# Optimization experiments

Measured on AMD Instinct MI355X. Metric: run time of the kernel, lower is better.

The kernel has to match this reference:

```python
import jax, jax.numpy as jnp
import numpy as np

N = 10000      # nodes per graph-batch
E = 160000     # edges
G = 128        # number of graphs (segments)


def gcn_conv(x, edge_index, W, b, n):
    """PyG GCNConv with normalize=True, add_self_loops=True.
    x: [n, in], W: [in, out], b: [out], edge_index: [2, e]."""
    loops = jnp.arange(n, dtype=edge_index.dtype)
    src = jnp.concatenate([edge_index[0], loops])
    dst = jnp.concatenate([edge_index[1], loops])
    deg = jnp.zeros((n,), x.dtype).at[dst].add(1.0)          # in-degree incl. self-loops
    dinv = jnp.where(deg > 0, jax.lax.rsqrt(deg), 0.0)
    norm = dinv[src] * dinv[dst]                              # [e+n]
    h = x @ W                                                 # dense transform first
    out = jax.ops.segment_sum(norm[:, None] * h[src], dst, num_segments=n)
    return out + b


def global_max_pool(z, batch, g):
    p = jax.ops.segment_max(z, batch, num_segments=g)
    return jnp.where(jnp.isneginf(p), 0.0, p)  # guard empty segments


def setup_inputs() -> dict:
    key = jax.random.key(0)
    ks = jax.random.split(key, 24)

    def w(k, i, o):
        return (jax.random.normal(k, (i, o), jnp.float32) / np.sqrt(i)).astype(jnp.float32)

    inp = {
        "x_s": jax.random.normal(ks[0], (N, 128), jnp.float32),
        "x_t": jax.random.normal(ks[1], (N, 128), jnp.float32),
        "edge_index_s": jax.random.randint(ks[2], (2, E), 0, N, dtype=jnp.int32),
        "edge_index_t": jax.random.randint(ks[3], (2, E), 0, N, dtype=jnp.int32),
        "xs_batch": jnp.sort(jax.random.randint(ks[4], (N,), 0, G, dtype=jnp.int32)),
        "xt_batch": jnp.sort(jax.random.randint(ks[5], (N,), 0, G, dtype=jnp.int32)),
        # encoder GCNConvs (128 -> 512)
        "W_enc1": w(ks[6], 128, 512), "b_enc1": jnp.zeros((512,), jnp.float32),
        "W_enc2": w(ks[7], 128, 512), "b_enc2": jnp.zeros((512,), jnp.float32),
        # branch-1 GCNConvs
        "W_r1g1": w(ks[8], 512, 1024), "b_r1g1": jnp.zeros((1024,), jnp.float32),
        "W_r1g2": w(ks[9], 1024, 2048), "b_r1g2": jnp.zeros((2048,), jnp.float32),
        # branch-2 GCNConvs
        "W_r2g1": w(ks[10], 512, 1024), "b_r2g1": jnp.zeros((1024,), jnp.float32),
        "W_r2g2": w(ks[11], 1024, 2048), "b_r2g2": jnp.zeros((2048,), jnp.float32),
        # MLP head
        "W_l1": w(ks[12], 2048, 1024), "b_l1": jnp.zeros((1024,), jnp.float32),
        "W_l2": w(ks[13], 1024, 1317), "b_l2": jnp.zeros((1317,), jnp.float32),
    }
    return inp


def reference(x_s, x_t, W_enc1, b_enc1, W_enc2, b_enc2,
              W_r1g1, b_r1g1, W_r1g2, b_r1g2,
              W_r2g1, b_r2g1, W_r2g2, b_r2g2,
              W_l1, b_l1, W_l2, b_l2,
              edge_index_s, edge_index_t, xs_batch, xt_batch):
    # branch 1 (source graphs)
    enc_r1 = gcn_conv(x_s, edge_index_s, W_enc1, b_enc1, N)
    z_r1 = jax.nn.relu(gcn_conv(enc_r1, edge_index_s, W_r1g1, b_r1g1, N))
    z_r1 = jax.nn.relu(gcn_conv(z_r1, edge_index_s, W_r1g2, b_r1g2, N))
    # branch 2 (target graphs)
    enc_r2 = gcn_conv(x_t, edge_index_t, W_enc2, b_enc2, N)
    z_r2 = jax.nn.relu(gcn_conv(enc_r2, edge_index_t, W_r2g1, b_r2g1, N))
    z_r2 = jax.nn.relu(gcn_conv(z_r2, edge_index_t, W_r2g2, b_r2g2, N))
    # global max pool per graph, then MLP head
    z = global_max_pool(z_r1, xs_batch, G) + global_max_pool(z_r2, xt_batch, G)  # [G, 2048]
    z = jax.nn.relu(z @ W_l1 + b_l1)
    z = z @ W_l2 + b_l2                                                          # [G, 1317]
    return (z, jax.nn.sigmoid(z))
```

## Files before the change

kernel.cpp:

```cpp
#include <hip/hip_runtime.h>
#include <cstdint>
#include <cstddef>


#define NN 10000
#define NNP 10112
#define MT 20224
#define NB 632
#define NE 160000
#define NG 128

typedef short bf16x8 __attribute__((ext_vector_type(8)));
typedef float f32x4 __attribute__((ext_vector_type(4)));

__device__ __forceinline__ unsigned short f2bf(float x) {
  unsigned u = __float_as_uint(x);
  u += 0x7FFFu + ((u >> 16) & 1u);
  return (unsigned short)(u >> 16);
}
__device__ __forceinline__ float bf2f(unsigned short h) {
  return __uint_as_float(((unsigned)h) << 16);
}
__device__ __forceinline__ void fma4(float4& d, float s, const float4& u) {
  d.x = fmaf(s, u.x, d.x);
  d.y = fmaf(s, u.y, d.y);
  d.z = fmaf(s, u.z, d.z);
  d.w = fmaf(s, u.w, d.w);
}

#define GLOAD_LDS16(gp, lp)                                                  \
  __builtin_amdgcn_global_load_lds(                                          \
      (const __attribute__((address_space(1))) void*)(gp),                   \
      (__attribute__((address_space(3))) void*)(lp), 16, 0, 0)


__global__ void k_count2(const int* __restrict__ eis, const int* __restrict__ eit,
                         int* __restrict__ cnt) {
  int i = blockIdx.x * blockDim.x + threadIdx.x;
  if (i >= 2 * NE) return;
  int d;
  if (i < NE) d = eis[NE + i];
  else        d = eit[NE + (i - NE)] + NNP;
  atomicAdd(&cnt[d], 1);
}

__global__ void k_scan(const int* __restrict__ cnt, int* __restrict__ row_ptr,
                       int* __restrict__ cursor, float* __restrict__ dinv,
                       const int* __restrict__ bs, const int* __restrict__ bt,
                       int* __restrict__ seg) {
  __shared__ int part[256];
  __shared__ int partex[257];
  int t = threadIdx.x;
  const int n = MT;
  const int CH = (n + 255) / 256;
  int base = t * CH;
  int s = 0;
  for (int i = 0; i < CH; ++i) {
    int idx = base + i;
    if (idx < n) s += cnt[idx];
  }
  part[t] = s;
  __syncthreads();
  if (t == 0) {
    int acc = 0;
    for (int i = 0; i < 256; ++i) { partex[i] = acc; acc += part[i]; }
    partex[256] = acc;
  }
  __syncthreads();
  int acc = partex[t];
  for (int i = 0; i < CH; ++i) {
    int idx = base + i;
    if (idx < n) {
      row_ptr[idx] = acc;
      cursor[idx]  = acc;
      dinv[idx] = rsqrtf((float)cnt[idx] + 1.0f);
      acc += cnt[idx];
    }
  }
  if (t == 255) row_ptr[n] = partex[256];
  if (t <= NG) {
    int lo = 0, hi = NN;
    while (lo < hi) {
      int mid = (lo + hi) >> 1;
      if (bs[mid] < t) lo = mid + 1;
      else hi = mid;
    }
    seg[t] = lo;
    lo = 0; hi = NN;
    while (lo < hi) {
      int mid = (lo + hi) >> 1;
      if (bt[mid] < t) lo = mid + 1;
      else hi = mid;
    }
    seg[(NG + 1) + t] = lo;
  }
}

__global__ void k_scatter2(const int* __restrict__ eis, const int* __restrict__ eit,
                           int* __restrict__ cursor, int* __restrict__ csr_src) {
  int i = blockIdx.x * blockDim.x + threadIdx.x;
  if (i >= 2 * NE) return;
  int s, d;
  if (i < NE) { s = eis[i]; d = eis[NE + i]; }
  else { int j = i - NE; s = eit[j] + NNP; d = eit[NE + j] + NNP; }
  int pos = atomicAdd(&cursor[d], 1);
  csr_src[pos] = s;
}

template <int NCH, bool DUAL>
__global__ __launch_bounds__(256) void k_agg_x(
    const float* __restrict__ in0, const float* __restrict__ in1,
    unsigned short* __restrict__ Ah, unsigned short* __restrict__ Al,
    const int* __restrict__ row_ptr, const int* __restrict__ csr_src,
    const float* __restrict__ dinv) {
  constexpr int F4TOT = NCH * 8;
  const int bid = blockIdx.x;
  const int xcd = bid & 7;
  const int seq = bid >> 3;
  int chunk, nodeblk;
  if constexpr (NCH >= 8) {
    int phase = seq / NB;
    nodeblk = seq - phase * NB;
    chunk = phase * 8 + xcd;
  } else {
    chunk = xcd >> 1;
    nodeblk = (seq << 1) | (xcd & 1);
  }
  const int t = threadIdx.x;
  const int node = nodeblk * 32 + (t >> 3);
  const int f4 = chunk * 8 + (t & 7);

  size_t o = (size_t)node * F4TOT + f4;
  ushort4* oh = (ushort4*)Ah + o;
  ushort4* ol = (ushort4*)Al + o;
  int local = (node < NNP) ? node : (node - NNP);
  if (local >= NN) {
    *oh = make_ushort4(0, 0, 0, 0);
    *ol = make_ushort4(0, 0, 0, 0);
    return;
  }
  const float4* i0 = (const float4*)in0;
  const float4* i1 = (const float4*)in1;
  auto rowp = [&](int g) -> const float4* {
    if (DUAL)
      return (g < NNP) ? (i0 + (size_t)g * F4TOT)
                       : (i1 + (size_t)(g - NNP) * F4TOT);
    return i0 + (size_t)g * F4TOT;
  };

  float di = dinv[node];
  float sw = di * di;
  float4 v = rowp(node)[f4];
  float4 acc;
  acc.x = sw * v.x; acc.y = sw * v.y; acc.z = sw * v.z; acc.w = sw * v.w;

  const int e0 = row_ptr[node], e1 = row_ptr[node + 1];
  int e = e0;
  for (; e + 4 <= e1; e += 4) {
    int s0 = csr_src[e], s1 = csr_src[e + 1];
    int s2 = csr_src[e + 2], s3 = csr_src[e + 3];
    float4 u0 = rowp(s0)[f4];
    float4 u1 = rowp(s1)[f4];
    float4 u2 = rowp(s2)[f4];
    float4 u3 = rowp(s3)[f4];
    float w0 = dinv[s0] * di, w1 = dinv[s1] * di;
    float w2 = dinv[s2] * di, w3 = dinv[s3] * di;
    fma4(acc, w0, u0);
    fma4(acc, w1, u1);
    fma4(acc, w2, u2);
    fma4(acc, w3, u3);
  }
  for (; e < e1; ++e) {
    int s = csr_src[e];
    float4 u = rowp(s)[f4];
    fma4(acc, dinv[s] * di, u);
  }

  ushort4 h, l;
  h.x = f2bf(acc.x); l.x = f2bf(acc.x - bf2f(h.x));
  h.y = f2bf(acc.y); l.y = f2bf(acc.y - bf2f(h.y));
  h.z = f2bf(acc.z); l.z = f2bf(acc.z - bf2f(h.z));
  h.w = f2bf(acc.w); l.w = f2bf(acc.w - bf2f(h.w));
  *oh = h;
  *ol = l;
}

__global__ __launch_bounds__(256) void k_wsplit2(
    const float* __restrict__ W0, unsigned short* __restrict__ H0,
    unsigned short* __restrict__ L0,
    const float* __restrict__ W1, unsigned short* __restrict__ H1,
    unsigned short* __restrict__ L1, int K, int N) {
  const float* W = blockIdx.z ? W1 : W0;
  unsigned short* Ht = blockIdx.z ? H1 : H0;
  unsigned short* Lt = blockIdx.z ? L1 : L0;
  __shared__ float tile[32][33];
  int nb = blockIdx.x * 32, kb = blockIdx.y * 32;
  int tx = threadIdx.x & 31, ty = threadIdx.x >> 5;
#pragma unroll
  for (int r = ty; r < 32; r += 8)
    tile[r][tx] = W[(size_t)(kb + r) * N + nb + tx];
  __syncthreads();
#pragma unroll
  for (int r = ty; r < 32; r += 8) {
    float x = tile[tx][r];
    unsigned short h = f2bf(x);
    unsigned short lo = f2bf(x - bf2f(h));
    size_t o = (size_t)(nb + r) * K + kb + tx;
    Ht[o] = h;
    Lt[o] = lo;
  }
}

template <bool RELU, int GX>
__global__ __launch_bounds__(256) void k_mgemm(
    const unsigned short* __restrict__ Ah, const unsigned short* __restrict__ Al,
    const unsigned short* __restrict__ Bh_a, const unsigned short* __restrict__ Bl_a,
    const unsigned short* __restrict__ Bh_b, const unsigned short* __restrict__ Bl_b,
    const float* __restrict__ bias_a, const float* __restrict__ bias_b,
    float* __restrict__ C, int N, int K, int AOFF) {
  __shared__ char smem[65536];
  const int t = threadIdx.x;
  const int w = t >> 6, l = t & 63;

  const int bid = blockIdx.x;
  int bn_, bm_;
  if constexpr (GX == 16) { bn_ = 2 * (bid & 7) + ((bid >> 3) & 1); bm_ = bid >> 4; }
  else if constexpr (GX == 8) { bn_ = bid & 7; bm_ = bid >> 3; }
  else { bn_ = bid & (GX - 1); bm_ = bid / GX; }
  const int bm = bm_ * 128, bn = bn_ * 128;
  const int arow = bm + AOFF;
  const bool sec = arow >= NNP;
  const unsigned short* Bh = sec ? Bh_b : Bh_a;
  const unsigned short* Bl = sec ? Bl_b : Bl_a;
  const float* bias = sec ? bias_b : bias_a;

  const int wr = w >> 1, wc = w & 1;

  f32x4 acc[4][4] = {};

  const unsigned short* g0 = (w == 0) ? Ah : (w == 1) ? Al : (w == 2) ? Bh : Bl;
  const int rb = (w < 2) ? arow : bn;
  const unsigned short* gbase = g0 + (size_t)(rb + (l & 15)) * K + ((l >> 4) * 8);
  const int sdoff = w * 8192 + l * 16;
  const int saoff = wr * 4096 + l * 16;
  const int sboff = 16384 + wc * 4096 + l * 16;

  const int nt = K >> 5;

#define STAGE(kt, b)                                                         \
  {                                                                          \
    const unsigned short* gk = gbase + ((kt) << 5);                          \
    char* sd = smem + (b)*32768 + sdoff;                                     \
    _Pragma("unroll") for (int s = 0; s < 8; ++s)                            \
        GLOAD_LDS16(gk + (size_t)s * 16 * K, sd + s * 1024);                 \
  }

  STAGE(0, 0)

  for (int kt = 0; kt < nt; ++kt) {
    const int cur = kt & 1;
    if (kt + 1 < nt) {
      STAGE(kt + 1, cur ^ 1)
      asm volatile("s_waitcnt vmcnt(8)" ::: "memory");
    } else {
      asm volatile("s_waitcnt vmcnt(0)" ::: "memory");
    }
    __builtin_amdgcn_sched_barrier(0);
    __builtin_amdgcn_s_barrier();

    const char* sA = smem + cur * 32768 + saoff;
    const char* sB = smem + cur * 32768 + sboff;
    bf16x8 a[4][2], b[4][2];
#pragma unroll
    for (int i = 0; i < 4; ++i) {
      a[i][0] = *(const bf16x8*)(sA + i * 1024);
      a[i][1] = *(const bf16x8*)(sA + 8192 + i * 1024);
    }
#pragma unroll
    for (int j = 0; j < 4; ++j) {
      b[j][0] = *(const bf16x8*)(sB + j * 1024);
      b[j][1] = *(const bf16x8*)(sB + 8192 + j * 1024);
    }
    asm volatile("s_waitcnt lgkmcnt(0)" ::: "memory");
    __builtin_amdgcn_sched_barrier(0);
    __builtin_amdgcn_s_barrier();

    __builtin_amdgcn_s_setprio(1);
#pragma unroll
    for (int i = 0; i < 4; ++i)
#pragma unroll
      for (int j = 0; j < 4; ++j) {
        acc[i][j] = __builtin_amdgcn_mfma_f32_16x16x32_bf16(a[i][0], b[j][0], acc[i][j], 0, 0, 0);
        acc[i][j] = __builtin_amdgcn_mfma_f32_16x16x32_bf16(a[i][0], b[j][1], acc[i][j], 0, 0, 0);
        acc[i][j] = __builtin_amdgcn_mfma_f32_16x16x32_bf16(a[i][1], b[j][0], acc[i][j], 0, 0, 0);
      }
    __builtin_amdgcn_s_setprio(0);
  }
#undef STAGE

  const int r0 = bm + wr * 64 + ((l >> 4) << 2);
  const int c0 = bn + wc * 64 + (l & 15);
#pragma unroll
  for (int j = 0; j < 4; ++j) {
    const int col = c0 + j * 16;
    const float bv = bias[col];
#pragma unroll
    for (int i = 0; i < 4; ++i) {
      const int row = r0 + i * 16;
#pragma unroll
      for (int r = 0; r < 4; ++r) {
        float v = acc[i][j][r] + bv;
        if (RELU) v = fmaxf(v, 0.f);
        C[(size_t)(row + r) * N + col] = v;
      }
    }
  }
}

__global__ __launch_bounds__(256) void k_gemm_sk(
    const float* __restrict__ A, const float* __restrict__ A2,
    const float* __restrict__ B,
    float* __restrict__ PART, int M, int N, int K, int KS) {
  __shared__ float As[32][64];
  __shared__ float Bs[32][64];

  int t = threadIdx.x;
  int tx = t & 15, ty = t >> 4;
  int bm = blockIdx.y * 64, bn = blockIdx.x * 64;
  int kbeg = blockIdx.z * KS, kend = kbeg + KS;

  float acc[4][4] = {};

  int arow0 = t >> 3;
  int ak4 = (t & 7) * 4;
  int brow0 = t >> 4;
  int bn4 = (t & 15) * 4;
  const bool n4al = (N & 3) == 0;

  for (int k0 = kbeg; k0 < kend; k0 += 32) {
#pragma unroll
    for (int c = 0; c < 2; ++c) {
      int row = arow0 + c * 32;
      int gr = bm + row;
      float4 v = make_float4(0.f, 0.f, 0.f, 0.f);
      if (gr < M) {
        v = *(const float4*)&A[(size_t)gr * K + k0 + ak4];
        if (A2) {
          float4 v2 = *(const float4*)&A2[(size_t)gr * K + k0 + ak4];
          v.x += v2.x; v.y += v2.y; v.z += v2.z; v.w += v2.w;
        }
      }
      As[ak4 + 0][row] = v.x;
      As[ak4 + 1][row] = v.y;
      As[ak4 + 2][row] = v.z;
      As[ak4 + 3][row] = v.w;
    }
#pragma unroll
    for (int c = 0; c < 2; ++c) {
      int row = brow0 + c * 16;
      int gc = bn + bn4;
      const float* bp = &B[(size_t)(k0 + row) * N + gc];
      float4 v;
      if (n4al && gc + 3 < N) {
        v = *(const float4*)bp;
      } else {
        v = make_float4(0.f, 0.f, 0.f, 0.f);
        if (gc < N) v.x = bp[0];
        if (gc + 1 < N) v.y = bp[1];
        if (gc + 2 < N) v.z = bp[2];
        if (gc + 3 < N) v.w = bp[3];
      }
      *(float4*)&Bs[row][bn4] = v;
    }
    __syncthreads();

#pragma unroll
    for (int kk = 0; kk < 32; ++kk) {
      float4 a = *(const float4*)&As[kk][ty * 4];
      float4 b = *(const float4*)&Bs[kk][tx * 4];
      float av[4] = {a.x, a.y, a.z, a.w};
      float bv[4] = {b.x, b.y, b.z, b.w};
#pragma unroll
      for (int i = 0; i < 4; ++i)
#pragma unroll
        for (int j = 0; j < 4; ++j)
          acc[i][j] = fmaf(av[i], bv[j], acc[i][j]);
    }
    __syncthreads();
  }

  float* P = PART + (size_t)blockIdx.z * M * N;
  int r0 = bm + ty * 4, c0 = bn + tx * 4;
#pragma unroll
  for (int i = 0; i < 4; ++i) {
    int r = r0 + i;
    if (r < M) {
#pragma unroll
      for (int j = 0; j < 4; ++j) {
        int c = c0 + j;
        if (c < N) P[(size_t)r * N + c] = acc[i][j];
      }
    }
  }
}

template <bool SIG>
__global__ void k_reduce(const float* __restrict__ PART,
                         const float* __restrict__ bias,
                         float* __restrict__ C, float* __restrict__ C2,
                         int MN, int N, int SK) {
  int i = blockIdx.x * blockDim.x + threadIdx.x;
  if (i >= MN) return;
  float s = 0.f;
  for (int z = 0; z < SK; ++z) s += PART[(size_t)z * MN + i];
  s += bias[i % N];
  if (SIG) {
    C[i] = s;
    C2[i] = 1.0f / (1.0f + __expf(-s));
  } else {
    C[i] = fmaxf(s, 0.f);
  }
}


__global__ void k_pool(const float* __restrict__ act, const int* __restrict__ segp,
                       float* __restrict__ P, int F4) {
  int g = blockIdx.x;
  int f4 = blockIdx.y * blockDim.x + threadIdx.x;
  if (f4 >= F4) return;
  const float4* a4 = (const float4*)act;
  int i0 = segp[g], i1 = segp[g + 1];
  float4 m = make_float4(0.f, 0.f, 0.f, 0.f);
  for (int i = i0; i < i1; ++i) {
    float4 u = a4[(size_t)i * F4 + f4];
    m.x = fmaxf(m.x, u.x);
    m.y = fmaxf(m.y, u.y);
    m.z = fmaxf(m.z, u.z);
    m.w = fmaxf(m.w, u.w);
  }
  ((float4*)P)[(size_t)g * F4 + f4] = m;
}


extern "C" void kernel_launch(void* const* d_in, const int* in_sizes, int n_in,
                              void* d_out, int out_size, void* d_ws, size_t ws_size,
                              hipStream_t stream) {
  const float* x_s = (const float*)d_in[0];
  const float* x_t = (const float*)d_in[1];
  const int* ei_s = (const int*)d_in[2];
  const int* ei_t = (const int*)d_in[3];
  const int* xs_batch = (const int*)d_in[4];
  const int* xt_batch = (const int*)d_in[5];
  const float* W_enc1 = (const float*)d_in[6];
  const float* b_enc1 = (const float*)d_in[7];
  const float* W_enc2 = (const float*)d_in[8];
  const float* b_enc2 = (const float*)d_in[9];
  const float* W_r1g1 = (const float*)d_in[10];
  const float* b_r1g1 = (const float*)d_in[11];
  const float* W_r1g2 = (const float*)d_in[12];
  const float* b_r1g2 = (const float*)d_in[13];
  const float* W_r2g1 = (const float*)d_in[14];
  const float* b_r2g1 = (const float*)d_in[15];
  const float* W_r2g2 = (const float*)d_in[16];
  const float* b_r2g2 = (const float*)d_in[17];
  const float* W_l1 = (const float*)d_in[18];
  const float* b_l1 = (const float*)d_in[19];
  const float* W_l2 = (const float*)d_in[20];
  const float* b_l2 = (const float*)d_in[21];

  float* out = (float*)d_out;

  char* ws = (char*)d_ws;
  size_t off = 0;
  auto carve = [&](size_t bytes) {
    char* p = ws + off;
    off = (off + bytes + 255) & ~(size_t)255;
    return p;
  };
  float* ACT = (float*)carve((size_t)MT * 1024 * 4);
  float* ACT3 = ACT;
  unsigned short* Ah = (unsigned short*)carve((size_t)MT * 1024 * 2);
  unsigned short* Al = (unsigned short*)carve((size_t)MT * 1024 * 2);
  unsigned short* W1h_a = (unsigned short*)carve((size_t)512 * 128 * 2);
  unsigned short* W1l_a = (unsigned short*)carve((size_t)512 * 128 * 2);
  unsigned short* W1h_b = (unsigned short*)carve((size_t)512 * 128 * 2);
  unsigned short* W1l_b = (unsigned short*)carve((size_t)512 * 128 * 2);
  unsigned short* W2h_a = (unsigned short*)carve((size_t)1024 * 512 * 2);
  unsigned short* W2l_a = (unsigned short*)carve((size_t)1024 * 512 * 2);
  unsigned short* W2h_b = (unsigned short*)carve((size_t)1024 * 512 * 2);
  unsigned short* W2l_b = (unsigned short*)carve((size_t)1024 * 512 * 2);
  unsigned short* W3h_a = (unsigned short*)carve((size_t)2048 * 1024 * 2);
  unsigned short* W3l_a = (unsigned short*)carve((size_t)2048 * 1024 * 2);
  unsigned short* W3h_b = (unsigned short*)carve((size_t)2048 * 1024 * 2);
  unsigned short* W3l_b = (unsigned short*)carve((size_t)2048 * 1024 * 2);
  float* P2   = (float*)carve((size_t)2 * NG * 2048 * 4);
  float* ZZ   = (float*)carve((size_t)NG * 1024 * 4);
  float* PART = (float*)carve((size_t)16 * NG * 1024 * 4);
  float* dinv = (float*)carve((size_t)MT * 4);
  int* cnt     = (int*)carve((size_t)MT * 4);
  int* row_ptr = (int*)carve((size_t)(MT + 1) * 4);
  int* cursor  = (int*)carve((size_t)MT * 4);
  int* csr_src = (int*)carve((size_t)2 * NE * 4);
  int* seg     = (int*)carve((size_t)2 * (NG + 1) * 4);
  (void)ws_size; (void)n_in; (void)in_sizes; (void)out_size;

  k_wsplit2<<<dim3(512 / 32, 128 / 32, 2), 256, 0, stream>>>(
      W_enc1, W1h_a, W1l_a, W_enc2, W1h_b, W1l_b, 128, 512);
  k_wsplit2<<<dim3(1024 / 32, 512 / 32, 2), 256, 0, stream>>>(
      W_r1g1, W2h_a, W2l_a, W_r2g1, W2h_b, W2l_b, 512, 1024);
  k_wsplit2<<<dim3(2048 / 32, 1024 / 32, 2), 256, 0, stream>>>(
      W_r1g2, W3h_a, W3l_a, W_r2g2, W3h_b, W3l_b, 1024, 2048);

  hipMemsetAsync(cnt, 0, (size_t)MT * 4, stream);
  k_count2<<<(2 * NE + 255) / 256, 256, 0, stream>>>(ei_s, ei_t, cnt);
  k_scan<<<1, 256, 0, stream>>>(cnt, row_ptr, cursor, dinv, xs_batch, xt_batch, seg);
  k_scatter2<<<(2 * NE + 255) / 256, 256, 0, stream>>>(ei_s, ei_t, cursor, csr_src);

  k_agg_x<4, true><<<NB * 4, 256, 0, stream>>>(
      x_s, x_t, Ah, Al, row_ptr, csr_src, dinv);
  k_mgemm<false, 4><<<4 * (MT / 128), 256, 0, stream>>>(
      Ah, Al, W1h_a, W1l_a, W1h_b, W1l_b, b_enc1, b_enc2, ACT, 512, 128, 0);

  k_agg_x<16, false><<<NB * 16, 256, 0, stream>>>(
      ACT, nullptr, Ah, Al, row_ptr, csr_src, dinv);
  k_mgemm<true, 8><<<8 * (MT / 128), 256, 0, stream>>>(
      Ah, Al, W2h_a, W2l_a, W2h_b, W2l_b, b_r1g1, b_r2g1, ACT, 1024, 512, 0);

  k_agg_x<32, false><<<NB * 32, 256, 0, stream>>>(
      ACT, nullptr, Ah, Al, row_ptr, csr_src, dinv);
  k_mgemm<true, 16><<<16 * (NNP / 128), 256, 0, stream>>>(
      Ah, Al, W3h_a, W3l_a, W3h_b, W3l_b, b_r1g2, b_r2g2, ACT3, 2048, 1024, 0);
  k_pool<<<dim3(NG, 2), 256, 0, stream>>>(ACT3, seg, P2, 512);
  k_mgemm<true, 16><<<16 * (NNP / 128), 256, 0, stream>>>(
      Ah, Al, W3h_a, W3l_a, W3h_b, W3l_b, b_r1g2, b_r2g2, ACT3, 2048, 1024, NNP);
  k_pool<<<dim3(NG, 2), 256, 0, stream>>>(ACT3, seg + (NG + 1),
                                          P2 + (size_t)NG * 2048, 512);

  k_gemm_sk<<<dim3(1024 / 64, 2, 16), 256, 0, stream>>>(
      P2, P2 + (size_t)NG * 2048, W_l1, PART, NG, 1024, 2048, 128);
  k_reduce<false><<<(NG * 1024 + 255) / 256, 256, 0, stream>>>(
      PART, b_l1, ZZ, nullptr, NG * 1024, 1024, 16);

  const int OUTN = 1317;
  k_gemm_sk<<<dim3((OUTN + 63) / 64, 2, 8), 256, 0, stream>>>(
      ZZ, nullptr, W_l2, PART, NG, OUTN, 1024, 128);
  k_reduce<true><<<(NG * OUTN + 255) / 256, 256, 0, stream>>>(
      PART, b_l2, out, out + (size_t)NG * OUTN, NG * OUTN, OUTN, 8);
}
```

Baseline: 835.2 us.

## Stage only hi bf16 halves in LDS; load lo halves directly from global

The split-bf16 GEMM now stages only the high halves of A and B in shared memory and halves the LDS footprint. The low halves are read straight from global memory into registers by each wave. The hand-tuned waitcnt, sched_barrier and setprio pipeline is replaced with plain __syncthreads. This aims to raise occupancy and cut LDS traffic, but the uncoalesced-ish per-wave global loads of lo halves and the coarser synchronisation could expose memory latency.

```diff
diff --git a/kernel.cpp b/kernel.cpp
--- a/kernel.cpp
+++ b/kernel.cpp
@@ -218,7 +218,7 @@
     const unsigned short* __restrict__ Bh_b, const unsigned short* __restrict__ Bl_b,
     const float* __restrict__ bias_a, const float* __restrict__ bias_b,
     float* __restrict__ C, int N, int K, int AOFF) {
-  __shared__ char smem[65536];
+  __shared__ char smem[32768];
   const int t = threadIdx.x;
   const int w = t >> 6, l = t & 63;
 
@@ -238,63 +238,59 @@
 
   f32x4 acc[4][4] = {};
 
-  const unsigned short* g0 = (w == 0) ? Ah : (w == 1) ? Al : (w == 2) ? Bh : Bl;
-  const int rb = (w < 2) ? arow : bn;
-  const unsigned short* gbase = g0 + (size_t)(rb + (l & 15)) * K + ((l >> 4) * 8);
-  const int sdoff = w * 8192 + l * 16;
+  const unsigned short* gmat = (w < 2) ? Ah : Bh;
+  const int rb0 = ((w < 2) ? arow : bn) + (w & 1) * 64;
+  const unsigned short* gsbase = gmat + (size_t)(rb0 + (l & 15)) * K + ((l >> 4) * 8);
+  const int sdoff = ((w < 2) ? 0 : 8192) + (w & 1) * 4096 + l * 16;
+
   const int saoff = wr * 4096 + l * 16;
-  const int sboff = 16384 + wc * 4096 + l * 16;
+  const int sboff = 8192 + wc * 4096 + l * 16;
+
+  const unsigned short* gal = Al + (size_t)(arow + wr * 64 + (l & 15)) * K + ((l >> 4) * 8);
+  const unsigned short* gbl = Bl + (size_t)(bn + wc * 64 + (l & 15)) * K + ((l >> 4) * 8);
 
   const int nt = K >> 5;
 
 #define STAGE(kt, b)                                                         \
   {                                                                          \
-    const unsigned short* gk = gbase + ((kt) << 5);                          \
-    char* sd = smem + (b)*32768 + sdoff;                                     \
-    _Pragma("unroll") for (int s = 0; s < 8; ++s)                            \
-        GLOAD_LDS16(gk + (size_t)s * 16 * K, sd + s * 1024);                 \
+    _Pragma("unroll") for (int s = 0; s < 4; ++s)                            \
+        GLOAD_LDS16(gsbase + (size_t)s * 16 * K + ((kt) << 5),               \
+                    smem + (b)*16384 + sdoff + s * 1024);                    \
   }
 
   STAGE(0, 0)
+  __syncthreads();
 
   for (int kt = 0; kt < nt; ++kt) {
     const int cur = kt & 1;
-    if (kt + 1 < nt) {
-      STAGE(kt + 1, cur ^ 1)
-      asm volatile("s_waitcnt vmcnt(8)" ::: "memory");
-    } else {
-      asm volatile("s_waitcnt vmcnt(0)" ::: "memory");
-    }
-    __builtin_amdgcn_sched_barrier(0);
-    __builtin_amdgcn_s_barrier();
-
-    const char* sA = smem + cur * 32768 + saoff;
-    const char* sB = smem + cur * 32768 + sboff;
-    bf16x8 a[4][2], b[4][2];
-#pragma unroll
-    for (int i = 0; i < 4; ++i) {
-      a[i][0] = *(const bf16x8*)(sA + i * 1024);
-      a[i][1] = *(const bf16x8*)(sA + 8192 + i * 1024);
-    }
-#pragma unroll
-    for (int j = 0; j < 4; ++j) {
-      b[j][0] = *(const bf16x8*)(sB + j * 1024);
-      b[j][1] = *(const bf16x8*)(sB + 8192 + j * 1024);
-    }
-    asm volatile("s_waitcnt lgkmcnt(0)" ::: "memory");
-    __builtin_amdgcn_sched_barrier(0);
-    __builtin_amdgcn_s_barrier();
-
-    __builtin_amdgcn_s_setprio(1);
+    if (kt + 1 < nt) STAGE(kt + 1, cur ^ 1)
+
+    const int k0 = kt << 5;
+    bf16x8 alo[4], blo[4];
 #pragma unroll
     for (int i = 0; i < 4; ++i)
+      alo[i] = *(const bf16x8*)(gal + (size_t)(i * 16) * K + k0);
+#pragma unroll
+    for (int j = 0; j < 4; ++j)
+      blo[j] = *(const bf16x8*)(gbl + (size_t)(j * 16) * K + k0);
+
+    const char* sA = smem + cur * 16384 + saoff;
+    const char* sB = smem + cur * 16384 + sboff;
+    bf16x8 ahi[4], bhi[4];
+#pragma unroll
+    for (int i = 0; i < 4; ++i) ahi[i] = *(const bf16x8*)(sA + i * 1024);
+#pragma unroll
+    for (int j = 0; j < 4; ++j) bhi[j] = *(const bf16x8*)(sB + j * 1024);
+
+#pragma unroll
+    for (int i = 0; i < 4; ++i)
 #pragma unroll
       for (int j = 0; j < 4; ++j) {
-        acc[i][j] = __builtin_amdgcn_mfma_f32_16x16x32_bf16(a[i][0], b[j][0], acc[i][j], 0, 0, 0);
-        acc[i][j] = __builtin_amdgcn_mfma_f32_16x16x32_bf16(a[i][0], b[j][1], acc[i][j], 0, 0, 0);
-        acc[i][j] = __builtin_amdgcn_mfma_f32_16x16x32_bf16(a[i][1], b[j][0], acc[i][j], 0, 0, 0);
+        acc[i][j] = __builtin_amdgcn_mfma_f32_16x16x32_bf16(ahi[i], bhi[j], acc[i][j], 0, 0, 0);
+        acc[i][j] = __builtin_amdgcn_mfma_f32_16x16x32_bf16(ahi[i], blo[j], acc[i][j], 0, 0, 0);
+        acc[i][j] = __builtin_amdgcn_mfma_f32_16x16x32_bf16(alo[i], bhi[j], acc[i][j], 0, 0, 0);
       }
-    __builtin_amdgcn_s_setprio(0);
+    __syncthreads();
   }
 #undef STAGE
 
```

Result: slower. 1.013 ms (+21.3%).

## Fuse final GCN GEMM with global max pool via atomicMax, 256x256 tiles

Applied to the files above, without the earlier changes.

Replaces the two half-size final-layer GEMM launches and their separate pool kernels with a single 256x256-tile, 512-thread GEMM. Its epilogue applies bias and ReLU, then atomically max-reduces into the pooled buffer using integer atomicMax on non-negative floats, so the 20k x 2048 activation is never written to or re-read from global memory. Node padding rises to 10240 so the larger tiles divide the rows, and the segment binary search in the scan kernel is dropped. The cost is atomic contention on the pooled buffer, a memset, some extra padded rows of work, and higher LDS and register pressure per block.

```diff
diff --git a/kernel.cpp b/kernel.cpp
--- a/kernel.cpp
+++ b/kernel.cpp
@@ -4,9 +4,9 @@
 
 
 #define NN 10000
-#define NNP 10112
-#define MT 20224
-#define NB 632
+#define NNP2 10240
+#define MT2 20480
+#define NB2 640
 #define NE 160000
 #define NG 128
 
@@ -40,25 +40,20 @@
   if (i >= 2 * NE) return;
   int d;
   if (i < NE) d = eis[NE + i];
-  else        d = eit[NE + (i - NE)] + NNP;
+  else        d = eit[NE + (i - NE)] + NNP2;
   atomicAdd(&cnt[d], 1);
 }
 
 __global__ void k_scan(const int* __restrict__ cnt, int* __restrict__ row_ptr,
-                       int* __restrict__ cursor, float* __restrict__ dinv,
-                       const int* __restrict__ bs, const int* __restrict__ bt,
-                       int* __restrict__ seg) {
+                       int* __restrict__ cursor, float* __restrict__ dinv) {
   __shared__ int part[256];
   __shared__ int partex[257];
   int t = threadIdx.x;
-  const int n = MT;
-  const int CH = (n + 255) / 256;
+  const int n = MT2;
+  const int CH = n / 256;
   int base = t * CH;
   int s = 0;
-  for (int i = 0; i < CH; ++i) {
-    int idx = base + i;
-    if (idx < n) s += cnt[idx];
-  }
+  for (int i = 0; i < CH; ++i) s += cnt[base + i];
   part[t] = s;
   __syncthreads();
   if (t == 0) {
@@ -70,30 +65,12 @@
   int acc = partex[t];
   for (int i = 0; i < CH; ++i) {
     int idx = base + i;
-    if (idx < n) {
-      row_ptr[idx] = acc;
-      cursor[idx]  = acc;
-      dinv[idx] = rsqrtf((float)cnt[idx] + 1.0f);
-      acc += cnt[idx];
-    }
+    row_ptr[idx] = acc;
+    cursor[idx]  = acc;
+    dinv[idx] = rsqrtf((float)cnt[idx] + 1.0f);
+    acc += cnt[idx];
   }
   if (t == 255) row_ptr[n] = partex[256];
-  if (t <= NG) {
-    int lo = 0, hi = NN;
-    while (lo < hi) {
-      int mid = (lo + hi) >> 1;
-      if (bs[mid] < t) lo = mid + 1;
-      else hi = mid;
-    }
-    seg[t] = lo;
-    lo = 0; hi = NN;
-    while (lo < hi) {
-      int mid = (lo + hi) >> 1;
-      if (bt[mid] < t) lo = mid + 1;
-      else hi = mid;
-    }
-    seg[(NG + 1) + t] = lo;
-  }
 }
 
 __global__ void k_scatter2(const int* __restrict__ eis, const int* __restrict__ eit,
@@ -102,7 +79,7 @@
   if (i >= 2 * NE) return;
   int s, d;
   if (i < NE) { s = eis[i]; d = eis[NE + i]; }
-  else { int j = i - NE; s = eit[j] + NNP; d = eit[NE + j] + NNP; }
+  else { int j = i - NE; s = eit[j] + NNP2; d = eit[NE + j] + NNP2; }
   int pos = atomicAdd(&cursor[d], 1);
   csr_src[pos] = s;
 }
@@ -119,8 +96,8 @@
   const int seq = bid >> 3;
   int chunk, nodeblk;
   if constexpr (NCH >= 8) {
-    int phase = seq / NB;
-    nodeblk = seq - phase * NB;
+    int phase = seq / NB2;
+    nodeblk = seq - phase * NB2;
     chunk = phase * 8 + xcd;
   } else {
     chunk = xcd >> 1;
@@ -133,7 +110,7 @@
   size_t o = (size_t)node * F4TOT + f4;
   ushort4* oh = (ushort4*)Ah + o;
   ushort4* ol = (ushort4*)Al + o;
-  int local = (node < NNP) ? node : (node - NNP);
+  int local = (node < NNP2) ? node : (node - NNP2);
   if (local >= NN) {
     *oh = make_ushort4(0, 0, 0, 0);
     *ol = make_ushort4(0, 0, 0, 0);
@@ -143,8 +120,8 @@
   const float4* i1 = (const float4*)in1;
   auto rowp = [&](int g) -> const float4* {
     if (DUAL)
-      return (g < NNP) ? (i0 + (size_t)g * F4TOT)
-                       : (i1 + (size_t)(g - NNP) * F4TOT);
+      return (g < NNP2) ? (i0 + (size_t)g * F4TOT)
+                        : (i1 + (size_t)(g - NNP2) * F4TOT);
     return i0 + (size_t)g * F4TOT;
   };
 
@@ -217,19 +194,15 @@
     const unsigned short* __restrict__ Bh_a, const unsigned short* __restrict__ Bl_a,
     const unsigned short* __restrict__ Bh_b, const unsigned short* __restrict__ Bl_b,
     const float* __restrict__ bias_a, const float* __restrict__ bias_b,
-    float* __restrict__ C, int N, int K, int AOFF) {
+    float* __restrict__ C, int N, int K) {
   __shared__ char smem[65536];
   const int t = threadIdx.x;
   const int w = t >> 6, l = t & 63;
 
   const int bid = blockIdx.x;
-  int bn_, bm_;
-  if constexpr (GX == 16) { bn_ = 2 * (bid & 7) + ((bid >> 3) & 1); bm_ = bid >> 4; }
-  else if constexpr (GX == 8) { bn_ = bid & 7; bm_ = bid >> 3; }
-  else { bn_ = bid & (GX - 1); bm_ = bid / GX; }
+  const int bn_ = bid & (GX - 1), bm_ = bid / GX;
   const int bm = bm_ * 128, bn = bn_ * 128;
-  const int arow = bm + AOFF;
-  const bool sec = arow >= NNP;
+  const bool sec = bm >= NNP2;
   const unsigned short* Bh = sec ? Bh_b : Bh_a;
   const unsigned short* Bl = sec ? Bl_b : Bl_a;
   const float* bias = sec ? bias_b : bias_a;
@@ -239,7 +212,7 @@
   f32x4 acc[4][4] = {};
 
   const unsigned short* g0 = (w == 0) ? Ah : (w == 1) ? Al : (w == 2) ? Bh : Bl;
-  const int rb = (w < 2) ? arow : bn;
+  const int rb = (w < 2) ? bm : bn;
   const unsigned short* gbase = g0 + (size_t)(rb + (l & 15)) * K + ((l >> 4) * 8);
   const int sdoff = w * 8192 + l * 16;
   const int saoff = wr * 4096 + l * 16;
@@ -312,6 +285,132 @@
         float v = acc[i][j][r] + bv;
         if (RELU) v = fmaxf(v, 0.f);
         C[(size_t)(row + r) * N + col] = v;
+      }
+    }
+  }
+}
+
+__global__ __launch_bounds__(512, 2) void k_mgemm3(
+    const unsigned short* __restrict__ Ah, const unsigned short* __restrict__ Al,
+    const unsigned short* __restrict__ Bh_a, const unsigned short* __restrict__ Bl_a,
+    const unsigned short* __restrict__ Bh_b, const unsigned short* __restrict__ Bl_b,
+    const float* __restrict__ bias_a, const float* __restrict__ bias_b,
+    const int* __restrict__ bs, const int* __restrict__ bt,
+    float* __restrict__ P2, int N, int K) {
+  __shared__ char smem[131072];
+  const int t = threadIdx.x;
+  const int w = t >> 6, l = t & 63;
+  const int bid = blockIdx.x;
+  const int bn_ = bid & 7, bm_ = bid >> 3;
+  const int bm = bm_ * 256, bn = bn_ * 256;
+  const bool sec = bm >= NNP2;
+  const unsigned short* Bh = sec ? Bh_b : Bh_a;
+  const unsigned short* Bl = sec ? Bl_b : Bl_a;
+  const float* bias = sec ? bias_b : bias_a;
+  const int* batch = sec ? bt : bs;
+  float* P2g = P2 + (sec ? (size_t)NG * 2048 : 0);
+  const int lbase = bm - (sec ? NNP2 : 0);
+
+  const int wr = w >> 2, wc = w & 3;
+
+  f32x4 acc[8][4] = {};
+
+  const int part = w >> 1, half = w & 1;
+  const unsigned short* gmat = (part == 0) ? Ah : (part == 1) ? Al
+                             : (part == 2) ? Bh : Bl;
+  const int rb = ((part < 2) ? bm : bn) + half * 128;
+  const unsigned short* gsbase = gmat + (size_t)(rb + (l & 15)) * K + ((l >> 4) * 8);
+  const int sdoff = part * 16384 + half * 8192 + l * 16;
+
+  const int saoff = (wr * 8) * 1024 + l * 16;
+  const int sboff = 32768 + (wc * 4) * 1024 + l * 16;
+
+  const int nt = K >> 5;
+
+#define STAGE3(kt, b)                                                        \
+  {                                                                          \
+    _Pragma("unroll") for (int c = 0; c < 8; ++c)                            \
+        GLOAD_LDS16(gsbase + (size_t)c * 16 * K + ((kt) << 5),               \
+                    smem + (b)*65536 + sdoff + c * 1024);                    \
+  }
+
+  STAGE3(0, 0)
+
+  for (int kt = 0; kt < nt; ++kt) {
+    const int cur = kt & 1;
+    if (kt + 1 < nt) {
+      STAGE3(kt + 1, cur ^ 1)
+      asm volatile("s_waitcnt vmcnt(8)" ::: "memory");
+    } else {
+      asm volatile("s_waitcnt vmcnt(0)" ::: "memory");
+    }
+    __builtin_amdgcn_sched_barrier(0);
+    __builtin_amdgcn_s_barrier();
+
+    const char* base = smem + cur * 65536;
+    bf16x8 bh[4], blo[4], ah[8], alo[8];
+#pragma unroll
+    for (int j = 0; j < 4; ++j) {
+      bh[j]  = *(const bf16x8*)(base + sboff + j * 1024);
+      blo[j] = *(const bf16x8*)(base + sboff + 16384 + j * 1024);
+    }
+#pragma unroll
+    for (int i = 0; i < 8; ++i) {
+      ah[i]  = *(const bf16x8*)(base + saoff + i * 1024);
+      alo[i] = *(const bf16x8*)(base + saoff + 16384 + i * 1024);
+    }
+    asm volatile("s_waitcnt lgkmcnt(0)" ::: "memory");
+    __builtin_amdgcn_sched_barrier(0);
+    __builtin_amdgcn_s_barrier();
+
+    __builtin_amdgcn_s_setprio(1);
+#pragma unroll
+    for (int i = 0; i < 8; ++i)
+#pragma unroll
+      for (int j = 0; j < 4; ++j) {
+        acc[i][j] = __builtin_amdgcn_mfma_f32_16x16x32_bf16(ah[i], bh[j], acc[i][j], 0, 0, 0);
+        acc[i][j] = __builtin_amdgcn_mfma_f32_16x16x32_bf16(ah[i], blo[j], acc[i][j], 0, 0, 0);
+        acc[i][j] = __builtin_amdgcn_mfma_f32_16x16x32_bf16(alo[i], bh[j], acc[i][j], 0, 0, 0);
+      }
+    __builtin_amdgcn_s_setprio(0);
+  }
+#undef STAGE3
+
+  const int r0l = lbase + wr * 128 + ((l >> 4) << 2);
+  const int c0 = bn + wc * 64 + (l & 15);
+#pragma unroll
+  for (int j = 0; j < 4; ++j) {
+    const int col = c0 + j * 16;
+    const float bv = bias[col];
+    float* Pcol = P2g + col;
+#pragma unroll
+    for (int i = 0; i < 8; ++i) {
+      const int rl = r0l + i * 16;
+      if (rl >= NN) continue;
+      float v0 = fmaxf(acc[i][j][0] + bv, 0.f);
+      float v1 = fmaxf(acc[i][j][1] + bv, 0.f);
+      float v2 = fmaxf(acc[i][j][2] + bv, 0.f);
+      float v3 = fmaxf(acc[i][j][3] + bv, 0.f);
+      if (rl + 3 < NN) {
+        int g0 = batch[rl], g3 = batch[rl + 3];
+        if (g0 == g3) {
+          float m = fmaxf(fmaxf(v0, v1), fmaxf(v2, v3));
+          atomicMax((int*)(Pcol + (size_t)g0 * 2048), __float_as_int(m));
+        } else {
+          int g1 = batch[rl + 1], g2 = batch[rl + 2];
+          atomicMax((int*)(Pcol + (size_t)g0 * 2048), __float_as_int(v0));
+          atomicMax((int*)(Pcol + (size_t)g1 * 2048), __float_as_int(v1));
+          atomicMax((int*)(Pcol + (size_t)g2 * 2048), __float_as_int(v2));
+          atomicMax((int*)(Pcol + (size_t)g3 * 2048), __float_as_int(v3));
+        }
+      } else {
+        float vv[4] = {v0, v1, v2, v3};
+        for (int r = 0; r < 4; ++r) {
+          if (rl + r < NN) {
+            int g = batch[rl + r];
+            atomicMax((int*)(Pcol + (size_t)g * 2048), __float_as_int(vv[r]));
+          }
+        }
       }
     }
   }
@@ -420,25 +519,6 @@
   } else {
     C[i] = fmaxf(s, 0.f);
   }
-}
-
-
-__global__ void k_pool(const float* __restrict__ act, const int* __restrict__ segp,
-                       float* __restrict__ P, int F4) {
-  int g = blockIdx.x;
-  int f4 = blockIdx.y * blockDim.x + threadIdx.x;
-  if (f4 >= F4) return;
-  const float4* a4 = (const float4*)act;
-  int i0 = segp[g], i1 = segp[g + 1];
-  float4 m = make_float4(0.f, 0.f, 0.f, 0.f);
-  for (int i = i0; i < i1; ++i) {
-    float4 u = a4[(size_t)i * F4 + f4];
-    m.x = fmaxf(m.x, u.x);
-    m.y = fmaxf(m.y, u.y);
-    m.z = fmaxf(m.z, u.z);
-    m.w = fmaxf(m.w, u.w);
-  }
-  ((float4*)P)[(size_t)g * F4 + f4] = m;
 }
 
 
@@ -477,10 +557,9 @@
     off = (off + bytes + 255) & ~(size_t)255;
     return p;
   };
-  float* ACT = (float*)carve((size_t)MT * 1024 * 4);
-  float* ACT3 = ACT;
-  unsigned short* Ah = (unsigned short*)carve((size_t)MT * 1024 * 2);
-  unsigned short* Al = (unsigned short*)carve((size_t)MT * 1024 * 2);
+  float* ACT = (float*)carve((size_t)MT2 * 1024 * 4);
+  unsigned short* Ah = (unsigned short*)carve((size_t)MT2 * 1024 * 2);
+  unsigned short* Al = (unsigned short*)carve((size_t)MT2 * 1024 * 2);
   unsigned short* W1h_a = (unsigned short*)carve((size_t)512 * 128 * 2);
   unsigned short* W1l_a = (unsigned short*)carve((size_t)512 * 128 * 2);
   unsigned short* W1h_b = (unsigned short*)carve((size_t)512 * 128 * 2);
@@ -496,12 +575,11 @@
   float* P2   = (float*)carve((size_t)2 * NG * 2048 * 4);
   float* ZZ   = (float*)carve((size_t)NG * 1024 * 4);
   float* PART = (float*)carve((size_t)16 * NG * 1024 * 4);
-  float* dinv = (float*)carve((size_t)MT * 4);
-  int* cnt     = (int*)carve((size_t)MT * 4);
-  int* row_ptr = (int*)carve((size_t)(MT + 1) * 4);
-  int* cursor  = (int*)carve((size_t)MT * 4);
+  float* dinv = (float*)carve((size_t)MT2 * 4);
+  int* cnt     = (int*)carve((size_t)MT2 * 4);
+  int* row_ptr = (int*)carve((size_t)(MT2 + 1) * 4);
+  int* cursor  = (int*)carve((size_t)MT2 * 4);
   int* csr_src = (int*)carve((size_t)2 * NE * 4);
-  int* seg     = (int*)carve((size_t)2 * (NG + 1) * 4);
   (void)ws_size; (void)n_in; (void)in_sizes; (void)out_size;
 
   k_wsplit2<<<dim3(512 / 32, 128 / 32, 2), 256, 0, stream>>>(
@@ -511,30 +589,27 @@
   k_wsplit2<<<dim3(2048 / 32, 1024 / 32, 2), 256, 0, stream>>>(
       W_r1g2, W3h_a, W3l_a, W_r2g2, W3h_b, W3l_b, 1024, 2048);
 
-  hipMemsetAsync(cnt, 0, (size_t)MT * 4, stream);
+  hipMemsetAsync(cnt, 0, (size_t)MT2 * 4, stream);
   k_count2<<<(2 * NE + 255) / 256, 256, 0, stream>>>(ei_s, ei_t, cnt);
-  k_scan<<<1, 256, 0, stream>>>(cnt, row_ptr, cursor, dinv, xs_batch, xt_batch, seg);
+  k_scan<<<1, 256, 0, stream>>>(cnt, row_ptr, cursor, dinv);
   k_scatter2<<<(2 * NE + 255) / 256, 256, 0, stream>>>(ei_s, ei_t, cursor, csr_src);
 
-  k_agg_x<4, true><<<NB * 4, 256, 0, stream>>>(
+  k_agg_x<4, true><<<NB2 * 4, 256, 0, stream>>>(
       x_s, x_t, Ah, Al, row_ptr, csr_src, dinv);
-  k_mgemm<false, 4><<<4 * (MT / 128), 256, 0, stream>>>(
-      Ah, Al, W1h_a, W1l_a, W1h_b, W1l_b, b_enc1, b_enc2, ACT, 512, 128, 0);
-
-  k_agg_x<16, false><<<NB * 16, 256, 0, stream>>>(
+  k_mgemm<false, 4><<<4 * (MT2 / 128), 256, 0, stream>>>(
+      Ah, Al, W1h_a, W1l_a, W1h_b, W1l_b, b_enc1, b_enc2, ACT, 512, 128);
+
+  k_agg_x<16, false><<<NB2 * 16, 256, 0, stream>>>(
       ACT, nullptr, Ah, Al, row_ptr, csr_src, dinv);
-  k_mgemm<true, 8><<<8 * (MT / 128), 256, 0, stream>>>(
-      Ah, Al, W2h_a, W2l_a, W2h_b, W2l_b, b_r1g1, b_r2g1, ACT, 1024, 512, 0);
-
-  k_agg_x<32, false><<<NB * 32, 256, 0, stream>>>(
+  k_mgemm<true, 8><<<8 * (MT2 / 128), 256, 0, stream>>>(
+      Ah, Al, W2h_a, W2l_a, W2h_b, W2l_b, b_r1g1, b_r2g1, ACT, 1024, 512);
+
+  k_agg_x<32, false><<<NB2 * 32, 256, 0, stream>>>(
       ACT, nullptr, Ah, Al, row_ptr, csr_src, dinv);
-  k_mgemm<true, 16><<<16 * (NNP / 128), 256, 0, stream>>>(
-      Ah, Al, W3h_a, W3l_a, W3h_b, W3l_b, b_r1g2, b_r2g2, ACT3, 2048, 1024, 0);
-  k_pool<<<dim3(NG, 2), 256, 0, stream>>>(ACT3, seg, P2, 512);
-  k_mgemm<true, 16><<<16 * (NNP / 128), 256, 0, stream>>>(
-      Ah, Al, W3h_a, W3l_a, W3h_b, W3l_b, b_r1g2, b_r2g2, ACT3, 2048, 1024, NNP);
-  k_pool<<<dim3(NG, 2), 256, 0, stream>>>(ACT3, seg + (NG + 1),
-                                          P2 + (size_t)NG * 2048, 512);
+  hipMemsetAsync(P2, 0, (size_t)2 * NG * 2048 * 4, stream);
+  k_mgemm3<<<8 * (MT2 / 256), 512, 0, stream>>>(
+      Ah, Al, W3h_a, W3l_a, W3h_b, W3l_b, b_r1g2, b_r2g2,
+      xs_batch, xt_batch, P2, 2048, 1024);
 
   k_gemm_sk<<<dim3(1024 / 64, 2, 16), 256, 0, stream>>>(
       P2, P2 + (size_t)NG * 2048, W_l1, PART, NG, 1024, 2048, 128);
```

After: 770.6 us. 7.7% less time.
